# Optimization experiments

Hardware: AMD Instinct MI355X
Metric: run time of the kernel (lower is better)

Reference implementation:

```python
import jax, jax.numpy as jnp
import numpy as np

L, B, IN, D, H, IN2D = 1024, 4, 256, 256, 8, 16
HD = D // H  # 32


def setup_inputs() -> dict:
    key = jax.random.key(0)
    ks = jax.random.split(key, 11)
    std = 0.02
    return {
        "s": jax.random.normal(ks[0], (L, B, IN), jnp.float32),
        "_k": jax.random.normal(ks[1], (L, B, IN), jnp.float32),
        "_v": jax.random.normal(ks[2], (L, B, IN), jnp.float32),
        "p": jax.random.normal(ks[3], (B, L, L, IN2D), jnp.float32),
        "Wq": jax.random.normal(ks[4], (IN, D), jnp.float32) * std,
        "Wk": jax.random.normal(ks[5], (IN, D), jnp.float32) * std,
        "Wv": jax.random.normal(ks[6], (IN, D), jnp.float32) * std,
        "Wo": jax.random.normal(ks[7], (D, IN), jnp.float32) * std,
        "bo": jax.random.normal(ks[8], (IN,), jnp.float32) * std,
        "W2d": jax.random.normal(ks[9], (H, IN2D), jnp.float32) * std,
        "b2d": jax.random.normal(ks[10], (H,), jnp.float32) * std,
    }


def reference(s, _k, _v, p, Wq, Wk, Wv, Wo, bo, W2d, b2d):
    # s: (L, B, IN); p: (B, L, L, IN2D)
    w_t = 1.0 / np.sqrt(D)  # dp_attn_norm == 'd_model'
    q = (s @ Wq).reshape(L, B, H, HD) * w_t
    k = (s @ Wk).reshape(L, B, H, HD)
    v = (s @ Wv).reshape(L, B, H, HD)
    # dot-product affinities: (B, H, L, L)
    scores = jnp.einsum('lbhd,mbhd->bhlm', q, k)
    # pairwise bias: mlp_2d(p) -> (B, L, L, H) -> (B, H, L, L)
    bias = jnp.einsum('bijc,hc->bhij', p, W2d) + b2d[None, :, None, None]
    attn = jax.nn.softmax(scores + bias, axis=-1)
    o = jnp.einsum('bhlm,mbhd->lbhd', attn, v).reshape(L, B, D)
    return (o @ Wo + bo,)
```

## Files before the change

### kernel.cpp

```cpp
#include <hip/hip_runtime.h>


typedef __attribute__((ext_vector_type(8))) short short8;
typedef __attribute__((ext_vector_type(4))) float f32x4;
typedef __attribute__((ext_vector_type(2))) _Float16 half2_t;
typedef unsigned short ushort_t;

#define JS_FIXED 4

__device__ inline unsigned short f2bf(float f) {
  unsigned int u = __float_as_uint(f);
  return (unsigned short)((u + 0x7FFFu + ((u >> 16) & 1u)) >> 16);
}

__global__ __launch_bounds__(256) void prep(
    const float* __restrict__ s, const float* __restrict__ Wq,
    const float* __restrict__ Wk, const float* __restrict__ Wv,
    const float* __restrict__ p, const float* __restrict__ W2d,
    const float* __restrict__ b2d,
    ushort_t* __restrict__ q_bf, ushort_t* __restrict__ k_bf, ushort_t* __restrict__ v_t,
    unsigned int* __restrict__ e16)
{
  __shared__ float s_lds[8][256];
  __shared__ unsigned int w2h[64];
  __shared__ float b2d_s[8];
  const int t = threadIdx.x;

  if (blockIdx.x < 512) {
    const int b = blockIdx.x >> 7;
    const int l0 = (blockIdx.x & 127) << 3;
    for (int rr = 0; rr < 8; ++rr)
      s_lds[rr][t] = s[((size_t)(((l0 + rr) << 2) + b) << 8) + t];
    __syncthreads();
    float aq[8], ak[8], av[8];
#pragma unroll
    for (int rr = 0; rr < 8; ++rr) { aq[rr] = 0.f; ak[rr] = 0.f; av[rr] = 0.f; }
    for (int k = 0; k < 256; ++k) {
      const float wq = Wq[k * 256 + t];
      const float wk = Wk[k * 256 + t];
      const float wv = Wv[k * 256 + t];
#pragma unroll
      for (int rr = 0; rr < 8; ++rr) {
        const float sv = s_lds[rr][k];
        aq[rr] = fmaf(sv, wq, aq[rr]);
        ak[rr] = fmaf(sv, wk, ak[rr]);
        av[rr] = fmaf(sv, wv, av[rr]);
      }
    }
    const int h = t >> 5, dl = t & 31;
#pragma unroll
    for (int rr = 0; rr < 8; ++rr) {
      const int l = l0 + rr;
      q_bf[(((size_t)(b << 10) + l) << 8) + t] = f2bf(aq[rr] * 0.0625f);
      k_bf[((((size_t)((b << 3) + h) << 10) + l) << 5) + dl] = f2bf(ak[rr]);
    }
    short8 vv;
#pragma unroll
    for (int rr = 0; rr < 8; ++rr) vv[rr] = (short)f2bf(av[rr]);
    *(short8*)&v_t[((((size_t)((b << 3) + h) << 5) + dl) << 10) + l0] = vv;
  } else {
    if (t < 64) {
      half2_t hv;
      hv[0] = (_Float16)W2d[2 * t];
      hv[1] = (_Float16)W2d[2 * t + 1];
      w2h[t] = __builtin_bit_cast(unsigned int, hv);
    }
    if (t < 8) b2d_s[t] = b2d[t];
    __syncthreads();

    const size_t base = (((size_t)blockIdx.x - 512) << 9);
    const size_t n0 = base + t;
    const size_t n1 = n0 + 256;

    const float4* p4 = (const float4*)p;
    float4 P0[4], P1[4];
#pragma unroll
    for (int c = 0; c < 4; ++c) P0[c] = p4[(n0 << 2) + c];
#pragma unroll
    for (int c = 0; c < 4; ++c) P1[c] = p4[(n1 << 2) + c];

    unsigned int w2r[64];
#pragma unroll
    for (int i = 0; i < 16; ++i) {
      const uint4 q = *(const uint4*)&w2h[i * 4];
      w2r[4 * i + 0] = q.x; w2r[4 * i + 1] = q.y;
      w2r[4 * i + 2] = q.z; w2r[4 * i + 3] = q.w;
    }
    float b2r[8];
#pragma unroll
    for (int h = 0; h < 8; ++h) b2r[h] = b2d_s[h];

#pragma unroll
    for (int pt = 0; pt < 2; ++pt) {
      const size_t n = pt ? n1 : n0;
      const float4* P = pt ? P1 : P0;
      unsigned int ph[8];
#pragma unroll
      for (int c = 0; c < 4; ++c) {
        unsigned int lo, hi;
        asm("v_cvt_pkrtz_f16_f32 %0, %1, %2" : "=v"(lo) : "v"(P[c].x), "v"(P[c].y));
        asm("v_cvt_pkrtz_f16_f32 %0, %1, %2" : "=v"(hi) : "v"(P[c].z), "v"(P[c].w));
        ph[2 * c] = lo; ph[2 * c + 1] = hi;
      }
      float acc[8];
#pragma unroll
      for (int h = 0; h < 8; ++h) {
        float a = b2r[h];
#pragma unroll
        for (int k = 0; k < 8; ++k)
          asm("v_dot2_f32_f16 %0, %1, %2, %0" : "+v"(a) : "v"(ph[k]), "v"(w2r[h * 8 + k]));
        acc[h] = a;
      }
      const int b = (int)(n >> 20);
      const unsigned int ij = (unsigned int)(n & 0xFFFFFu);
#pragma unroll
      for (int w = 0; w < 4; ++w) {
        half2_t hv;
        hv[0] = (_Float16)acc[2 * w];
        hv[1] = (_Float16)acc[2 * w + 1];
        e16[(((size_t)((b << 2) + w)) << 20) + ij] = __builtin_bit_cast(unsigned int, hv);
      }
    }
  }
}

template <int JS>
__global__ __launch_bounds__(256, 4) void attn_mfma(
    const ushort_t* __restrict__ q_bf, const ushort_t* __restrict__ k_bf,
    const ushort_t* __restrict__ v_t, const unsigned int* __restrict__ ep,
    float* __restrict__ o_part, float* __restrict__ lsum_part)
{
  __shared__ __align__(16) ushort_t p_lds[2][8][16][40];

  const int t = threadIdx.x;
  const int flat = blockIdx.x + (blockIdx.y << 6) + (blockIdx.z << 8);
  const int swz = ((flat & 7) << 7) + (flat >> 3);
  const int i0 = (swz & 63) << 4;
  const int b  = (swz >> 6) & 3;
  const int js = swz >> 8;

  const int w = t >> 6;
  const int l = t & 63;
  const int lrow = l & 15;
  const int lgrp = l >> 4;

  short8 qa[2];
#pragma unroll
  for (int h2 = 0; h2 < 2; ++h2) {
    const int h = (w << 1) + h2;
    qa[h2] = *(const short8*)&q_bf[(((size_t)(b << 10) + i0 + lrow) << 8) + (h << 5) + (lgrp << 3)];
  }

  f32x4 o_acc[2][2];
  float ls[2][4];
#pragma unroll
  for (int h2 = 0; h2 < 2; ++h2) {
#pragma unroll
    for (int nh = 0; nh < 2; ++nh) o_acc[h2][nh] = (f32x4){0.f, 0.f, 0.f, 0.f};
#pragma unroll
    for (int r = 0; r < 4; ++r) ls[h2][r] = 0.f;
  }

  const size_t A0 = (((size_t)((b << 2) + w)) << 20) + ((size_t)(i0 + (lgrp << 2)) << 10) + lrow;

  auto LOADE = [&](int j0, unsigned int (&ub)[2][4]) {
#pragma unroll
    for (int jh = 0; jh < 2; ++jh)
#pragma unroll
      for (int r = 0; r < 4; ++r)
        ub[jh][r] = ep[A0 + ((size_t)r << 10) + (jh << 4) + j0];
  };

  auto COMPUTE = [&](int j0, unsigned int (&ub)[2][4], int pb) {
#pragma unroll
    for (int jh = 0; jh < 2; ++jh) {
#pragma unroll
      for (int h2 = 0; h2 < 2; ++h2) {
        const int h = (w << 1) + h2;
        const short8 kb = *(const short8*)&k_bf[((((size_t)((b << 3) + h) << 10) + j0 + (jh << 4) + lrow) << 5) + (lgrp << 3)];
        f32x4 cc;
#pragma unroll
        for (int r = 0; r < 4; ++r) {
          const half2_t hv = __builtin_bit_cast(half2_t, ub[jh][r]);
          cc[r] = (float)hv[h2];
        }
        f32x4 d = __builtin_amdgcn_mfma_f32_16x16x32_bf16(qa[h2], kb, cc, 0, 0, 0);
#pragma unroll
        for (int r = 0; r < 4; ++r) {
          const float ex = __expf(d[r]);
          ls[h2][r] += ex;
          p_lds[pb][h][(lgrp << 2) + r][(jh << 4) + lrow] = f2bf(ex);
        }
      }
    }
#pragma unroll
    for (int h2 = 0; h2 < 2; ++h2) {
      const int h = (w << 1) + h2;
      const short8 pa = *(const short8*)&p_lds[pb][h][lrow][lgrp << 3];
#pragma unroll
      for (int nh = 0; nh < 2; ++nh) {
        const short8 vb = *(const short8*)&v_t[((((size_t)((b << 3) + h) << 5) + (nh << 4) + lrow) << 10) + j0 + (lgrp << 3)];
        o_acc[h2][nh] = __builtin_amdgcn_mfma_f32_16x16x32_bf16(pa, vb, o_acc[h2][nh], 0, 0, 0);
      }
    }
  };

  constexpr int CHUNK = 1024 / JS;
  constexpr int NT = CHUNK / 32;
  const int jbeg = js * CHUNK;
  const int jlast = jbeg + CHUNK - 32;

  unsigned int ubA[2][4], ubB[2][4];
  LOADE(jbeg, ubA);
#pragma unroll 1
  for (int t2 = 0; t2 < NT; t2 += 2) {
    const int j0 = jbeg + (t2 << 5);
    const int jn1 = (j0 + 32 < jlast) ? (j0 + 32) : jlast;
    const int jn2 = (j0 + 64 < jlast) ? (j0 + 64) : jlast;
    LOADE(jn1, ubB);
    COMPUTE(j0, ubA, 0);
    LOADE(jn2, ubA);
    COMPUTE(j0 + 32, ubB, 1);
  }

#pragma unroll
  for (int h2 = 0; h2 < 2; ++h2) {
#pragma unroll
    for (int r = 0; r < 4; ++r) {
      float v = ls[h2][r];
      v += __shfl_xor(v, 1, 16);
      v += __shfl_xor(v, 2, 16);
      v += __shfl_xor(v, 4, 16);
      v += __shfl_xor(v, 8, 16);
      ls[h2][r] = v;
    }
  }
  const size_t obase = ((size_t)js << 20) + (((size_t)(b << 10) + i0) << 8);
#pragma unroll
  for (int h2 = 0; h2 < 2; ++h2) {
    const int h = (w << 1) + h2;
#pragma unroll
    for (int nh = 0; nh < 2; ++nh) {
      const int d = (h << 5) + (nh << 4) + lrow;
#pragma unroll
      for (int r = 0; r < 4; ++r)
        o_part[obase + ((size_t)((lgrp << 2) + r) << 8) + d] = o_acc[h2][nh][r];
    }
  }
  if (lrow == 0) {
#pragma unroll
    for (int h2 = 0; h2 < 2; ++h2) {
      const int h = (w << 1) + h2;
      float* lp = lsum_part + (((size_t)((js << 5) + (b << 3) + h)) << 10) + i0;
#pragma unroll
      for (int r = 0; r < 4; ++r)
        lp[(lgrp << 2) + r] = ls[h2][r];
    }
  }
}

__global__ __launch_bounds__(256) void out_proj(
    const float* __restrict__ o_part, const float* __restrict__ lsum_part,
    const float* __restrict__ Wo, const float* __restrict__ bo,
    float* __restrict__ out)
{
  constexpr int JS = JS_FIXED;
  __shared__ float o_lds[8][256];
  const int t = threadIdx.x;
  const int r0 = blockIdx.x << 3;
  const int h = t >> 5;
  for (int rr = 0; rr < 8; ++rr) {
    const int r = r0 + rr;
    const int l = r >> 2, bb = r & 3;
    const size_t base = (((size_t)(bb << 10) + l) << 8) + t;
    float acc = 0.f;
#pragma unroll
    for (int js = 0; js < JS; ++js)
      acc += o_part[((size_t)js << 20) + base];
    float lsv = 0.f;
#pragma unroll
    for (int js = 0; js < JS; ++js)
      lsv += lsum_part[(((size_t)((js << 5) + (bb << 3) + h)) << 10) + l];
    o_lds[rr][t] = acc / lsv;
  }
  __syncthreads();
  float accs[8];
#pragma unroll
  for (int rr = 0; rr < 8; ++rr) accs[rr] = 0.f;
  for (int k = 0; k < 256; ++k) {
    const float wo = Wo[k * 256 + t];
#pragma unroll
    for (int rr = 0; rr < 8; ++rr)
      accs[rr] = fmaf(o_lds[rr][k], wo, accs[rr]);
  }
  const float bov = bo[t];
#pragma unroll
  for (int rr = 0; rr < 8; ++rr)
    out[(size_t)(r0 + rr) * 256 + t] = accs[rr] + bov;
}

extern "C" void kernel_launch(void* const* d_in, const int* in_sizes, int n_in,
                              void* d_out, int out_size, void* d_ws, size_t ws_size,
                              hipStream_t stream)
{
  const float* s   = (const float*)d_in[0];
  const float* p   = (const float*)d_in[3];
  const float* Wq  = (const float*)d_in[4];
  const float* Wk  = (const float*)d_in[5];
  const float* Wv  = (const float*)d_in[6];
  const float* Wo  = (const float*)d_in[7];
  const float* bo  = (const float*)d_in[8];
  const float* W2d = (const float*)d_in[9];
  const float* b2d = (const float*)d_in[10];
  float* out = (float*)d_out;

  ushort_t* q_bf = (ushort_t*)d_ws;
  ushort_t* k_bf = q_bf + (1 << 20);
  ushort_t* v_t  = k_bf + (1 << 20);
  unsigned int* e16 = (unsigned int*)(v_t + (1 << 20));
  float* o_part = (float*)((char*)e16 + ((size_t)1 << 26));
  float* lsum_part = o_part + ((size_t)JS_FIXED << 20);

  prep<<<dim3(512 + 8192), dim3(256), 0, stream>>>(s, Wq, Wk, Wv, p, W2d, b2d,
                                                   q_bf, k_bf, v_t, e16);
  attn_mfma<JS_FIXED><<<dim3(64, 4, JS_FIXED), dim3(256), 0, stream>>>(
      q_bf, k_bf, v_t, e16, o_part, lsum_part);
  out_proj<<<dim3(512), dim3(256), 0, stream>>>(o_part, lsum_part, Wo, bo, out);
}
```

Before: 139.6 us.

## Make bias-prep blocks persistent with double-buffered nontemporal loads of p

The pairwise-bias part of the prep kernel now has each block process 4096 positions in a loop of 16 chunks instead of 512 positions, cutting the grid from 8192 to 1024 bias blocks. Loads of p are software-pipelined: the next chunk is fetched into a second register set while the current one is converted and dotted. The loads use nontemporal hints so the 268 MB stream of p does not pollute cache. This amortizes the per-block W2d setup and aims to keep more memory requests in flight, at the cost of fewer blocks and more registers per thread.

```diff
diff --git a/kernel.cpp b/kernel.cpp
--- a/kernel.cpp
+++ b/kernel.cpp
@@ -68,17 +68,6 @@
     if (t < 8) b2d_s[t] = b2d[t];
     __syncthreads();
 
-    const size_t base = (((size_t)blockIdx.x - 512) << 9);
-    const size_t n0 = base + t;
-    const size_t n1 = n0 + 256;
-
-    const float4* p4 = (const float4*)p;
-    float4 P0[4], P1[4];
-#pragma unroll
-    for (int c = 0; c < 4; ++c) P0[c] = p4[(n0 << 2) + c];
-#pragma unroll
-    for (int c = 0; c < 4; ++c) P1[c] = p4[(n1 << 2) + c];
-
     unsigned int w2r[64];
 #pragma unroll
     for (int i = 0; i < 16; ++i) {
@@ -90,17 +79,25 @@
 #pragma unroll
     for (int h = 0; h < 8; ++h) b2r[h] = b2d_s[h];
 
-#pragma unroll
-    for (int pt = 0; pt < 2; ++pt) {
-      const size_t n = pt ? n1 : n0;
-      const float4* P = pt ? P1 : P0;
+    const size_t base = ((size_t)(blockIdx.x - 512)) << 12;
+    const f32x4* p4 = (const f32x4*)p;
+
+    f32x4 PA[4], PB[4];
+    auto LOADP = [&](int c, f32x4 (&R)[4]) {
+      const size_t n = base + ((size_t)c << 8) + t;
+#pragma unroll
+      for (int cc = 0; cc < 4; ++cc)
+        R[cc] = __builtin_nontemporal_load(&p4[(n << 2) + cc]);
+    };
+    auto DOPT = [&](int c, f32x4 (&R)[4]) {
+      const size_t n = base + ((size_t)c << 8) + t;
       unsigned int ph[8];
 #pragma unroll
-      for (int c = 0; c < 4; ++c) {
+      for (int cc = 0; cc < 4; ++cc) {
         unsigned int lo, hi;
-        asm("v_cvt_pkrtz_f16_f32 %0, %1, %2" : "=v"(lo) : "v"(P[c].x), "v"(P[c].y));
-        asm("v_cvt_pkrtz_f16_f32 %0, %1, %2" : "=v"(hi) : "v"(P[c].z), "v"(P[c].w));
-        ph[2 * c] = lo; ph[2 * c + 1] = hi;
+        asm("v_cvt_pkrtz_f16_f32 %0, %1, %2" : "=v"(lo) : "v"(R[cc][0]), "v"(R[cc][1]));
+        asm("v_cvt_pkrtz_f16_f32 %0, %1, %2" : "=v"(hi) : "v"(R[cc][2]), "v"(R[cc][3]));
+        ph[2 * cc] = lo; ph[2 * cc + 1] = hi;
       }
       float acc[8];
 #pragma unroll
@@ -120,6 +117,15 @@
         hv[1] = (_Float16)acc[2 * w + 1];
         e16[(((size_t)((b << 2) + w)) << 20) + ij] = __builtin_bit_cast(unsigned int, hv);
       }
+    };
+
+    LOADP(0, PA);
+#pragma unroll 1
+    for (int c = 0; c < 16; c += 2) {
+      LOADP(c + 1, PB);
+      DOPT(c, PA);
+      if (c + 2 < 16) LOADP(c + 2, PA);
+      DOPT(c + 1, PB);
     }
   }
 }
@@ -321,7 +327,7 @@
   float* o_part = (float*)((char*)e16 + ((size_t)1 << 26));
   float* lsum_part = o_part + ((size_t)JS_FIXED << 20);
 
-  prep<<<dim3(512 + 8192), dim3(256), 0, stream>>>(s, Wq, Wk, Wv, p, W2d, b2d,
+  prep<<<dim3(512 + 1024), dim3(256), 0, stream>>>(s, Wq, Wk, Wv, p, W2d, b2d,
                                                    q_bf, k_bf, v_t, e16);
   attn_mfma<JS_FIXED><<<dim3(64, 4, JS_FIXED), dim3(256), 0, stream>>>(
       q_bf, k_bf, v_t, e16, o_part, lsum_part);
```

Result: slower. 160.0 us (+14.6%).
